# Optimization experiments

Measured on AMD Instinct MI355X. Metric: run time of the kernel, lower is better.

The kernel has to match this reference:

```python
import jax, jax.numpy as jnp
import numpy as np

N_NODES = 100000


def sage_conv(x, src, dst, w_self, w_neigh, b):
    # DGL SAGEConv with 'mean' aggregator: out = x @ W_self + mean_neigh(x) @ W_neigh + b
    msg = x[src]                                                     # [E, d] gather
    agg = jax.ops.segment_sum(msg, dst, num_segments=N_NODES)        # [N, d]
    deg = jax.ops.segment_sum(jnp.ones((src.shape[0],), x.dtype), dst,
                              num_segments=N_NODES)                  # [N]
    h_neigh = agg / jnp.maximum(deg, 1.0)[:, None]                   # mean; 0 for isolated nodes
    return x @ w_self + h_neigh @ w_neigh + b


def setup_inputs() -> dict:
    key = jax.random.key(0)
    ks = jax.random.split(key, 12)
    N, E = N_NODES, 1600000
    in_f, h_f, r_f = 128, 128, 64
    glorot = lambda k, i, o: jax.random.normal(k, (i, o), jnp.float32) / np.float32(np.sqrt(i))
    return {
        "in_feat": jax.random.normal(ks[0], (N, in_f), jnp.float32),
        "src": jax.random.randint(ks[1], (E,), 0, N),
        "dst": jax.random.randint(ks[2], (E,), 0, N),
        "w1_self": glorot(ks[3], in_f, h_f), "w1_neigh": glorot(ks[4], in_f, h_f), "b1": jnp.zeros((h_f,), jnp.float32),
        "w2_self": glorot(ks[5], h_f, r_f), "w2_neigh": glorot(ks[6], h_f, r_f), "b2": jnp.zeros((r_f,), jnp.float32),
        "w3_self": glorot(ks[7], r_f, r_f), "w3_neigh": glorot(ks[8], r_f, r_f), "b3": jnp.zeros((r_f,), jnp.float32),
    }


def reference(in_feat, src, dst,
              w1_self, w1_neigh, b1,
              w2_self, w2_neigh, b2,
              w3_self, w3_neigh, b3):
    h = sage_conv(in_feat, src, dst, w1_self, w1_neigh, b1)
    h = jax.nn.relu(h)
    h = sage_conv(h, src, dst, w2_self, w2_neigh, b2)
    h = jax.nn.relu(h)
    # dropout is treated as identity (deterministic eval-mode reference)
    h = sage_conv(h, src, dst, w3_self, w3_neigh, b3)
    return jax.nn.softmax(h, axis=-1)
```

## Files before the change

kernel.cpp:

```cpp
#include <hip/hip_runtime.h>
#include <hip/hip_bf16.h>

#define N_NODES 100000

typedef unsigned short ushort_t;
typedef __attribute__((ext_vector_type(8))) short short8;
typedef __attribute__((ext_vector_type(4))) float f32x4;

static __device__ __forceinline__ ushort_t f2bf(float f) {
    unsigned u = __float_as_uint(f);
    unsigned r = u + 0x7FFFu + ((u >> 16) & 1u);
    return (ushort_t)(r >> 16);
}
static __device__ __forceinline__ float bf2f(ushort_t h) {
    return __uint_as_float(((unsigned)h) << 16);
}

static __device__ __forceinline__ void split8(const float* __restrict__ xp,
                                              short8& hi, short8& lo) {
    float4 x0 = *(const float4*)xp;
    float4 x1 = *(const float4*)(xp + 4);
    float xs[8] = {x0.x, x0.y, x0.z, x0.w, x1.x, x1.y, x1.z, x1.w};
    #pragma unroll
    for (int j = 0; j < 8; ++j) {
        ushort_t h = f2bf(xs[j]);
        hi[j] = (short)h;
        lo[j] = (short)f2bf(xs[j] - bf2f(h));
    }
}

__global__ __launch_bounds__(256) void hist_kernel(const int* __restrict__ dst,
                                                   int* __restrict__ deg, int E) {
    int e = blockIdx.x * 256 + threadIdx.x;
    if (e < E) atomicAdd(&deg[__builtin_nontemporal_load(&dst[e])], 1);
}

__global__ __launch_bounds__(256) void scan_partial_sums(const int* __restrict__ deg,
                                                         int* __restrict__ partials, int N) {
    __shared__ int wsums[4];
    int tid = threadIdx.x, lane = tid & 63, wv = tid >> 6;
    int i0 = blockIdx.x * 1024 + tid * 4;
    int s = 0;
    #pragma unroll
    for (int j = 0; j < 4; ++j) {
        int i = i0 + j;
        if (i < N) s += deg[i];
    }
    #pragma unroll
    for (int off = 32; off > 0; off >>= 1) s += __shfl_xor(s, off, 64);
    if (lane == 0) wsums[wv] = s;
    __syncthreads();
    if (tid == 0)
        partials[blockIdx.x] = wsums[0] + wsums[1] + wsums[2] + wsums[3];
}

__global__ __launch_bounds__(256) void scan_partials(int* __restrict__ partials, int NB,
                                                     int* __restrict__ row_ptr, int N) {
    __shared__ int wsums[4];
    int tid = threadIdx.x, lane = tid & 63, wv = tid >> 6;
    int v = (tid < NB) ? partials[tid] : 0;
    int x = v;
    #pragma unroll
    for (int off = 1; off < 64; off <<= 1) {
        int y = __shfl_up(x, off, 64);
        if (lane >= off) x += y;
    }
    if (lane == 63) wsums[wv] = x;
    __syncthreads();
    int woff = 0;
    for (int w = 0; w < wv; ++w) woff += wsums[w];
    int incl = x + woff;
    if (tid < NB) partials[tid] = incl - v;
    if (tid == NB - 1) row_ptr[N] = incl;
}

__global__ __launch_bounds__(256) void scan_emit(const int* __restrict__ deg,
                                                 const int* __restrict__ partials,
                                                 int* __restrict__ row_ptr,
                                                 int* __restrict__ cursor,
                                                 float* __restrict__ inv_deg,
                                                 int* __restrict__ gcur, int N) {
    __shared__ int wsums[4];
    int tid = threadIdx.x, lane = tid & 63, wv = tid >> 6;
    int i0 = blockIdx.x * 1024 + tid * 4;
    int d[4];
    #pragma unroll
    for (int j = 0; j < 4; ++j) {
        int i = i0 + j;
        d[j] = (i < N) ? deg[i] : 0;
    }
    int s = d[0] + d[1] + d[2] + d[3];
    int x = s;
    #pragma unroll
    for (int off = 1; off < 64; off <<= 1) {
        int y = __shfl_up(x, off, 64);
        if (lane >= off) x += y;
    }
    if (lane == 63) wsums[wv] = x;
    __syncthreads();
    int woff = 0;
    for (int w = 0; w < wv; ++w) woff += wsums[w];
    int run = partials[blockIdx.x] + woff + x - s;
    #pragma unroll
    for (int j = 0; j < 4; ++j) {
        int i = i0 + j;
        if (i < N) {
            row_ptr[i] = run;
            cursor[i]  = run;
            inv_deg[i] = 1.0f / (float)(d[j] > 0 ? d[j] : 1);
            if ((i & 255) == 0) gcur[i >> 8] = run;
            run += d[j];
        }
    }
}

#define MAXBUCK 512
__global__ __launch_bounds__(256) void bin_pairs(const int* __restrict__ src,
                                                 const int* __restrict__ dst,
                                                 int* __restrict__ gcur,
                                                 long long* __restrict__ staged,
                                                 int E, int NBUCK, int C) {
    __shared__ int cnt[MAXBUCK];
    int tid = threadIdx.x;
    int e0 = blockIdx.x * C;
    int e1 = min(e0 + C, E);
    for (int b = tid; b < NBUCK; b += 256) cnt[b] = 0;
    __syncthreads();
    for (int e = e0 + tid; e < e1; e += 256) {
        int d = __builtin_nontemporal_load(&dst[e]);
        atomicAdd(&cnt[d >> 8], 1);
    }
    __syncthreads();
    for (int b = tid; b < NBUCK; b += 256) {
        int c = cnt[b];
        cnt[b] = (c > 0) ? atomicAdd(&gcur[b], c) : 0;
    }
    __syncthreads();
    for (int e = e0 + tid; e < e1; e += 256) {
        int d = __builtin_nontemporal_load(&dst[e]);
        int s = __builtin_nontemporal_load(&src[e]);
        int p = atomicAdd(&cnt[d >> 8], 1);
        staged[p] = ((long long)d << 32) | (unsigned)s;
    }
}

__global__ __launch_bounds__(256) void scatter_bucket(const long long* __restrict__ staged,
                                                      const int* __restrict__ row_ptr,
                                                      int* __restrict__ cursor,
                                                      int* __restrict__ edge_src,
                                                      int N) {
    int b = blockIdx.x;
    int lo = b << 8;
    int hiN = min((b + 1) << 8, N);
    int gstart = row_ptr[lo];
    int gend   = row_ptr[hiN];
    for (int p = gstart + threadIdx.x; p < gend; p += 256) {
        long long pr = __builtin_nontemporal_load(&staged[p]);
        int d = (int)(pr >> 32);
        int s = (int)(pr & 0xFFFFFFFFll);
        int pos = atomicAdd(&cursor[d], 1);
        edge_src[pos] = s;
    }
}

__global__ __launch_bounds__(256) void pack_all(
        const float* __restrict__ W0, const float* __restrict__ W1,
        const float* __restrict__ W2, const float* __restrict__ W3,
        const float* __restrict__ W4, const float* __restrict__ W5,
        ushort_t* H0, ushort_t* L0, ushort_t* H1, ushort_t* L1,
        ushort_t* H2, ushort_t* L2, ushort_t* H3, ushort_t* L3,
        ushort_t* H4, ushort_t* L4, ushort_t* H5, ushort_t* L5) {
    int b = blockIdx.x;
    const float* W; ushort_t* Hi; ushort_t* Lo; int K, NS, base;
    if (b < 8)       { W = W0; Hi = H0; Lo = L0; K = 128; NS = 128; base = 0;  }
    else if (b < 16) { W = W1; Hi = H1; Lo = L1; K = 128; NS = 128; base = 8;  }
    else if (b < 20) { W = W2; Hi = H2; Lo = L2; K = 128; NS = 64;  base = 16; }
    else if (b < 24) { W = W3; Hi = H3; Lo = L3; K = 128; NS = 64;  base = 20; }
    else if (b < 26) { W = W4; Hi = H4; Lo = L4; K = 64;  NS = 64;  base = 24; }
    else             { W = W5; Hi = H5; Lo = L5; K = 64;  NS = 64;  base = 26; }
    int tid = (b - base) * 256 + threadIdx.x;
    if (tid >= (K * NS) / 8) return;
    int l  = tid & 63;
    int fl = tid >> 6;
    int NT = NS / 16;
    int t = fl % NT, s = fl / NT;
    ushort_t hs[8], ls[8];
    #pragma unroll
    for (int j = 0; j < 8; ++j) {
        int k = s * 32 + (l >> 4) * 8 + j;
        int n = t * 16 + (l & 15);
        float w = W[(size_t)k * NS + n];
        ushort_t h = f2bf(w);
        hs[j] = h;
        ls[j] = f2bf(w - bf2f(h));
    }
    #pragma unroll
    for (int j = 0; j < 8; ++j) {
        Hi[(size_t)tid * 8 + j] = hs[j];
        Lo[(size_t)tid * 8 + j] = ls[j];
    }
}

template <int K, int NS>
__global__ __launch_bounds__(256) void mfma_gemm(const float* __restrict__ X,
                                                 const ushort_t* __restrict__ BsHi,
                                                 const ushort_t* __restrict__ BsLo,
                                                 const ushort_t* __restrict__ BnHi,
                                                 const ushort_t* __restrict__ BnLo,
                                                 const float* __restrict__ bias,
                                                 float* __restrict__ S,
                                                 ushort_t* __restrict__ Zb,
                                                 int M) {
    constexpr int KS = K / 32;
    constexpr int NT = NS / 16;
    __shared__ float ldsS[4][32 * 20];
    __shared__ float ldsZ[4][32 * 20];
    int tid = threadIdx.x;
    int lane = tid & 63, w = tid >> 6;
    int baseM = blockIdx.x * 128 + w * 32;
    int rIn = lane & 15, q = lane >> 4;
    float* bufS = ldsS[w];
    float* bufZ = ldsZ[w];

    short8 Ahi[KS][2], Alo[KS][2];
    #pragma unroll
    for (int s = 0; s < KS; ++s) {
        #pragma unroll
        for (int mt = 0; mt < 2; ++mt) {
            int gm = baseM + mt * 16 + rIn;
            if (gm < M) {
                split8(&X[(size_t)gm * K + s * 32 + q * 8], Ahi[s][mt], Alo[s][mt]);
            } else {
                #pragma unroll
                for (int j = 0; j < 8; ++j) { Ahi[s][mt][j] = 0; Alo[s][mt][j] = 0; }
            }
        }
    }

    for (int t = 0; t < NT; ++t) {
        f32x4 aS0 = {0.f, 0.f, 0.f, 0.f}, aS1 = {0.f, 0.f, 0.f, 0.f};
        f32x4 aZ0 = {0.f, 0.f, 0.f, 0.f}, aZ1 = {0.f, 0.f, 0.f, 0.f};
        #pragma unroll
        for (int s = 0; s < KS; ++s) {
            size_t fo = ((size_t)(s * NT + t) * 64 + lane) * 8;
            short8 bsh = *(const short8*)&BsHi[fo];
            short8 bsl = *(const short8*)&BsLo[fo];
            short8 bnh = *(const short8*)&BnHi[fo];
            short8 bnl = *(const short8*)&BnLo[fo];
            aS0 = __builtin_amdgcn_mfma_f32_16x16x32_bf16(Ahi[s][0], bsh, aS0, 0, 0, 0);
            aS0 = __builtin_amdgcn_mfma_f32_16x16x32_bf16(Alo[s][0], bsh, aS0, 0, 0, 0);
            aS0 = __builtin_amdgcn_mfma_f32_16x16x32_bf16(Ahi[s][0], bsl, aS0, 0, 0, 0);
            aS1 = __builtin_amdgcn_mfma_f32_16x16x32_bf16(Ahi[s][1], bsh, aS1, 0, 0, 0);
            aS1 = __builtin_amdgcn_mfma_f32_16x16x32_bf16(Alo[s][1], bsh, aS1, 0, 0, 0);
            aS1 = __builtin_amdgcn_mfma_f32_16x16x32_bf16(Ahi[s][1], bsl, aS1, 0, 0, 0);
            aZ0 = __builtin_amdgcn_mfma_f32_16x16x32_bf16(Ahi[s][0], bnh, aZ0, 0, 0, 0);
            aZ0 = __builtin_amdgcn_mfma_f32_16x16x32_bf16(Alo[s][0], bnh, aZ0, 0, 0, 0);
            aZ0 = __builtin_amdgcn_mfma_f32_16x16x32_bf16(Ahi[s][0], bnl, aZ0, 0, 0, 0);
            aZ1 = __builtin_amdgcn_mfma_f32_16x16x32_bf16(Ahi[s][1], bnh, aZ1, 0, 0, 0);
            aZ1 = __builtin_amdgcn_mfma_f32_16x16x32_bf16(Alo[s][1], bnh, aZ1, 0, 0, 0);
            aZ1 = __builtin_amdgcn_mfma_f32_16x16x32_bf16(Ahi[s][1], bnl, aZ1, 0, 0, 0);
        }
        #pragma unroll
        for (int r = 0; r < 4; ++r) {
            bufS[(q * 4 + r) * 20 + rIn]        = aS0[r];
            bufS[(16 + q * 4 + r) * 20 + rIn]   = aS1[r];
            bufZ[(q * 4 + r) * 20 + rIn]        = aZ0[r];
            bufZ[(16 + q * 4 + r) * 20 + rIn]   = aZ1[r];
        }
        int row = lane >> 2;
        int cq  = lane & 3;
        int col = t * 16 + cq * 4;
        float4 bv = *(const float4*)&bias[col];
        #pragma unroll
        for (int half = 0; half < 2; ++half) {
            int gm = baseM + half * 16 + row;
            float4 v = *(float4*)&bufS[(half * 16 + row) * 20 + cq * 4];
            float4 z = *(float4*)&bufZ[(half * 16 + row) * 20 + cq * 4];
            if (gm < M) {
                float4 o;
                o.x = v.x + bv.x; o.y = v.y + bv.y;
                o.z = v.z + bv.z; o.w = v.w + bv.w;
                *(float4*)&S[(size_t)gm * NS + col] = o;
                uint2 o2;
                o2.x = (unsigned)f2bf(z.x) | ((unsigned)f2bf(z.y) << 16);
                o2.y = (unsigned)f2bf(z.z) | ((unsigned)f2bf(z.w) << 16);
                *(uint2*)&Zb[(size_t)gm * NS + col] = o2;
            }
        }
    }
}

template <int D, int ACT>
__global__ __launch_bounds__(256) void agg_kernel(const float* __restrict__ S,
                                                  const uint2* __restrict__ Zu,
                                                  const int* __restrict__ row_ptr,
                                                  const int* __restrict__ edge_src,
                                                  const float* __restrict__ inv_deg,
                                                  float* __restrict__ out, int N) {
    constexpr int G  = D / 4;
    constexpr int NG = 256 / G;
    int tid = threadIdx.x;
    int g = tid / G, f4 = tid % G;
    int n = blockIdx.x * NG + g;
    if (n >= N) return;
    int beg = row_ptr[n], end = row_ptr[n + 1];

    float a0[4] = {0, 0, 0, 0}, a1[4] = {0, 0, 0, 0};
    float a2[4] = {0, 0, 0, 0}, a3[4] = {0, 0, 0, 0};
#define ACC(u, a)                                                              \
    a[0] += __uint_as_float((u).x << 16);                                      \
    a[1] += __uint_as_float((u).x & 0xFFFF0000u);                              \
    a[2] += __uint_as_float((u).y << 16);                                      \
    a[3] += __uint_as_float((u).y & 0xFFFF0000u);
    int j = beg;
    for (; j + 3 < end; j += 4) {
        int s0 = edge_src[j + 0], s1 = edge_src[j + 1];
        int s2 = edge_src[j + 2], s3 = edge_src[j + 3];
        uint2 u0 = Zu[(size_t)s0 * G + f4];
        uint2 u1 = Zu[(size_t)s1 * G + f4];
        uint2 u2 = Zu[(size_t)s2 * G + f4];
        uint2 u3 = Zu[(size_t)s3 * G + f4];
        ACC(u0, a0) ACC(u1, a1) ACC(u2, a2) ACC(u3, a3)
    }
    for (; j < end; ++j) {
        uint2 u = Zu[(size_t)edge_src[j] * G + f4];
        ACC(u, a0)
    }
#undef ACC
    float id = inv_deg[n];
    float4 sv = ((const float4*)(S + (size_t)n * D))[f4];
    float v[4];
    v[0] = sv.x + id * ((a0[0] + a1[0]) + (a2[0] + a3[0]));
    v[1] = sv.y + id * ((a0[1] + a1[1]) + (a2[1] + a3[1]));
    v[2] = sv.z + id * ((a0[2] + a1[2]) + (a2[2] + a3[2]));
    v[3] = sv.w + id * ((a0[3] + a1[3]) + (a2[3] + a3[3]));

    float4 o;
    if (ACT == 0) {
        o.x = fmaxf(v[0], 0.f); o.y = fmaxf(v[1], 0.f);
        o.z = fmaxf(v[2], 0.f); o.w = fmaxf(v[3], 0.f);
    } else {
        float m = fmaxf(fmaxf(v[0], v[1]), fmaxf(v[2], v[3]));
        #pragma unroll
        for (int off = 8; off > 0; off >>= 1) m = fmaxf(m, __shfl_xor(m, off, 16));
        float e0 = __expf(v[0] - m), e1 = __expf(v[1] - m);
        float e2 = __expf(v[2] - m), e3 = __expf(v[3] - m);
        float s = (e0 + e1) + (e2 + e3);
        #pragma unroll
        for (int off = 8; off > 0; off >>= 1) s += __shfl_xor(s, off, 16);
        float inv = 1.0f / s;
        o.x = e0 * inv; o.y = e1 * inv; o.z = e2 * inv; o.w = e3 * inv;
    }
    ((float4*)(out + (size_t)n * D))[f4] = o;
}

extern "C" void kernel_launch(void* const* d_in, const int* in_sizes, int n_in,
                              void* d_out, int out_size, void* d_ws, size_t ws_size,
                              hipStream_t stream) {
    const float* in_feat = (const float*)d_in[0];
    const int*   src     = (const int*)d_in[1];
    const int*   dst     = (const int*)d_in[2];
    const float* w1s = (const float*)d_in[3];
    const float* w1n = (const float*)d_in[4];
    const float* b1  = (const float*)d_in[5];
    const float* w2s = (const float*)d_in[6];
    const float* w2n = (const float*)d_in[7];
    const float* b2  = (const float*)d_in[8];
    const float* w3s = (const float*)d_in[9];
    const float* w3n = (const float*)d_in[10];
    const float* b3  = (const float*)d_in[11];

    const int N = N_NODES;
    const int E = in_sizes[1];

    char* p = (char*)d_ws;
    auto carve = [&](size_t bytes) -> char* {
        char* q = p;
        p += (bytes + 511) & ~(size_t)511;
        return q;
    };
    float*    S        = (float*)   carve((size_t)N * 128 * sizeof(float));
    ushort_t* Zb       = (ushort_t*)carve((size_t)N * 128 * sizeof(ushort_t));
    float*    H        = (float*)   carve((size_t)N * 128 * sizeof(float));
    int*      edge_src = (int*)     carve((size_t)E * sizeof(int));
    int*      row_ptr  = (int*)     carve((size_t)(N + 1) * sizeof(int));
    int*      cursor   = (int*)     carve((size_t)N * sizeof(int));
    int*      deg      = (int*)     carve((size_t)N * sizeof(int));
    float*    invd     = (float*)   carve((size_t)N * sizeof(float));
    int*      partials = (int*)     carve(256 * sizeof(int));
    int*      gcur     = (int*)     carve(MAXBUCK * sizeof(int));
    long long* staged  = (long long*)H;
    ushort_t* P1sH = (ushort_t*)carve(128 * 128 * 2); ushort_t* P1sL = (ushort_t*)carve(128 * 128 * 2);
    ushort_t* P1nH = (ushort_t*)carve(128 * 128 * 2); ushort_t* P1nL = (ushort_t*)carve(128 * 128 * 2);
    ushort_t* P2sH = (ushort_t*)carve(128 * 64 * 2);  ushort_t* P2sL = (ushort_t*)carve(128 * 64 * 2);
    ushort_t* P2nH = (ushort_t*)carve(128 * 64 * 2);  ushort_t* P2nL = (ushort_t*)carve(128 * 64 * 2);
    ushort_t* P3sH = (ushort_t*)carve(64 * 64 * 2);   ushort_t* P3sL = (ushort_t*)carve(64 * 64 * 2);
    ushort_t* P3nH = (ushort_t*)carve(64 * 64 * 2);   ushort_t* P3nL = (ushort_t*)carve(64 * 64 * 2);

    pack_all<<<28, 256, 0, stream>>>(w1s, w1n, w2s, w2n, w3s, w3n,
                                     P1sH, P1sL, P1nH, P1nL,
                                     P2sH, P2sL, P2nH, P2nL,
                                     P3sH, P3sL, P3nH, P3nL);

    (void)hipMemsetAsync(deg, 0, (size_t)N * sizeof(int), stream);
    hist_kernel<<<(E + 255) / 256, 256, 0, stream>>>(dst, deg, E);
    const int NB = (N + 1023) / 1024;
    scan_partial_sums<<<NB, 256, 0, stream>>>(deg, partials, N);
    scan_partials<<<1, 256, 0, stream>>>(partials, NB, row_ptr, N);
    scan_emit<<<NB, 256, 0, stream>>>(deg, partials, row_ptr, cursor, invd, gcur, N);
    const int NBUCK = (N + 255) >> 8;
    const int BINB  = 256;
    const int CHUNK = (E + BINB - 1) / BINB;
    bin_pairs<<<BINB, 256, 0, stream>>>(src, dst, gcur, staged, E, NBUCK, CHUNK);
    scatter_bucket<<<NBUCK, 256, 0, stream>>>(staged, row_ptr, cursor, edge_src, N);

    const int GB = (N + 127) / 128;

    mfma_gemm<128, 128><<<GB, 256, 0, stream>>>(in_feat, P1sH, P1sL, P1nH, P1nL, b1, S, Zb, N);
    agg_kernel<128, 0><<<(N + 7) / 8, 256, 0, stream>>>(S, (const uint2*)Zb,
                                                        row_ptr, edge_src, invd, H, N);

    mfma_gemm<128, 64><<<GB, 256, 0, stream>>>(H, P2sH, P2sL, P2nH, P2nL, b2, S, Zb, N);
    agg_kernel<64, 0><<<(N + 15) / 16, 256, 0, stream>>>(S, (const uint2*)Zb,
                                                         row_ptr, edge_src, invd, H, N);

    mfma_gemm<64, 64><<<GB, 256, 0, stream>>>(H, P3sH, P3sL, P3nH, P3nL, b3, S, Zb, N);
    agg_kernel<64, 1><<<(N + 15) / 16, 256, 0, stream>>>(S, (const uint2*)Zb,
                                                         row_ptr, edge_src, invd,
                                                         (float*)d_out, N);
}
```

Baseline: 474.6 us.

## Fuse setup kernels, store hidden activations in bf16, widen aggregation vectors

Merges weight packing with the degree histogram, and the bucket scatter with the first GEMM, into single launches so independent work shares one grid. Hidden activations between layers are now stored as bf16, and the later GEMMs use a single-term A operand (two MFMAs per tile instead of three), which cuts memory traffic and MFMA count. The aggregation kernel now reads 8 bf16 features per thread with uint4 loads and uses nontemporal loads for edge indices and S. The cost is lower precision on intermediate activations and a separate staging buffer that no longer aliases H.

```diff
diff --git a/kernel.cpp b/kernel.cpp
--- a/kernel.cpp
+++ b/kernel.cpp
@@ -29,10 +29,48 @@
     }
 }
 
-__global__ __launch_bounds__(256) void hist_kernel(const int* __restrict__ dst,
-                                                   int* __restrict__ deg, int E) {
-    int e = blockIdx.x * 256 + threadIdx.x;
-    if (e < E) atomicAdd(&deg[__builtin_nontemporal_load(&dst[e])], 1);
+__global__ __launch_bounds__(256) void pack_hist(
+        const float* __restrict__ W0, const float* __restrict__ W1,
+        const float* __restrict__ W2, const float* __restrict__ W3,
+        const float* __restrict__ W4, const float* __restrict__ W5,
+        ushort_t* H0, ushort_t* L0, ushort_t* H1, ushort_t* L1,
+        ushort_t* H2, ushort_t* L2, ushort_t* H3, ushort_t* L3,
+        ushort_t* H4, ushort_t* L4, ushort_t* H5, ushort_t* L5,
+        const int* __restrict__ dst, int* __restrict__ deg, int E) {
+    int b = blockIdx.x;
+    if (b >= 28) {
+        int e = (b - 28) * 256 + threadIdx.x;
+        if (e < E) atomicAdd(&deg[__builtin_nontemporal_load(&dst[e])], 1);
+        return;
+    }
+    const float* W; ushort_t* Hi; ushort_t* Lo; int K, NS, base;
+    if (b < 8)       { W = W0; Hi = H0; Lo = L0; K = 128; NS = 128; base = 0;  }
+    else if (b < 16) { W = W1; Hi = H1; Lo = L1; K = 128; NS = 128; base = 8;  }
+    else if (b < 20) { W = W2; Hi = H2; Lo = L2; K = 128; NS = 64;  base = 16; }
+    else if (b < 24) { W = W3; Hi = H3; Lo = L3; K = 128; NS = 64;  base = 20; }
+    else if (b < 26) { W = W4; Hi = H4; Lo = L4; K = 64;  NS = 64;  base = 24; }
+    else             { W = W5; Hi = H5; Lo = L5; K = 64;  NS = 64;  base = 26; }
+    int tid = (b - base) * 256 + threadIdx.x;
+    if (tid >= (K * NS) / 8) return;
+    int l  = tid & 63;
+    int fl = tid >> 6;
+    int NT = NS / 16;
+    int t = fl % NT, s = fl / NT;
+    ushort_t hs[8], ls[8];
+    #pragma unroll
+    for (int j = 0; j < 8; ++j) {
+        int k = s * 32 + (l >> 4) * 8 + j;
+        int n = t * 16 + (l & 15);
+        float w = W[(size_t)k * NS + n];
+        ushort_t h = f2bf(w);
+        hs[j] = h;
+        ls[j] = f2bf(w - bf2f(h));
+    }
+    #pragma unroll
+    for (int j = 0; j < 8; ++j) {
+        Hi[(size_t)tid * 8 + j] = hs[j];
+        Lo[(size_t)tid * 8 + j] = ls[j];
+    }
 }
 
 __global__ __launch_bounds__(256) void scan_partial_sums(const int* __restrict__ deg,
@@ -144,80 +182,38 @@
     }
 }
 
-__global__ __launch_bounds__(256) void scatter_bucket(const long long* __restrict__ staged,
-                                                      const int* __restrict__ row_ptr,
-                                                      int* __restrict__ cursor,
-                                                      int* __restrict__ edge_src,
-                                                      int N) {
-    int b = blockIdx.x;
-    int lo = b << 8;
-    int hiN = min((b + 1) << 8, N);
-    int gstart = row_ptr[lo];
-    int gend   = row_ptr[hiN];
-    for (int p = gstart + threadIdx.x; p < gend; p += 256) {
-        long long pr = __builtin_nontemporal_load(&staged[p]);
-        int d = (int)(pr >> 32);
-        int s = (int)(pr & 0xFFFFFFFFll);
-        int pos = atomicAdd(&cursor[d], 1);
-        edge_src[pos] = s;
-    }
-}
-
-__global__ __launch_bounds__(256) void pack_all(
-        const float* __restrict__ W0, const float* __restrict__ W1,
-        const float* __restrict__ W2, const float* __restrict__ W3,
-        const float* __restrict__ W4, const float* __restrict__ W5,
-        ushort_t* H0, ushort_t* L0, ushort_t* H1, ushort_t* L1,
-        ushort_t* H2, ushort_t* L2, ushort_t* H3, ushort_t* L3,
-        ushort_t* H4, ushort_t* L4, ushort_t* H5, ushort_t* L5) {
-    int b = blockIdx.x;
-    const float* W; ushort_t* Hi; ushort_t* Lo; int K, NS, base;
-    if (b < 8)       { W = W0; Hi = H0; Lo = L0; K = 128; NS = 128; base = 0;  }
-    else if (b < 16) { W = W1; Hi = H1; Lo = L1; K = 128; NS = 128; base = 8;  }
-    else if (b < 20) { W = W2; Hi = H2; Lo = L2; K = 128; NS = 64;  base = 16; }
-    else if (b < 24) { W = W3; Hi = H3; Lo = L3; K = 128; NS = 64;  base = 20; }
-    else if (b < 26) { W = W4; Hi = H4; Lo = L4; K = 64;  NS = 64;  base = 24; }
-    else             { W = W5; Hi = H5; Lo = L5; K = 64;  NS = 64;  base = 26; }
-    int tid = (b - base) * 256 + threadIdx.x;
-    if (tid >= (K * NS) / 8) return;
-    int l  = tid & 63;
-    int fl = tid >> 6;
-    int NT = NS / 16;
-    int t = fl % NT, s = fl / NT;
-    ushort_t hs[8], ls[8];
-    #pragma unroll
-    for (int j = 0; j < 8; ++j) {
-        int k = s * 32 + (l >> 4) * 8 + j;
-        int n = t * 16 + (l & 15);
-        float w = W[(size_t)k * NS + n];
-        ushort_t h = f2bf(w);
-        hs[j] = h;
-        ls[j] = f2bf(w - bf2f(h));
-    }
-    #pragma unroll
-    for (int j = 0; j < 8; ++j) {
-        Hi[(size_t)tid * 8 + j] = hs[j];
-        Lo[(size_t)tid * 8 + j] = ls[j];
-    }
-}
-
-template <int K, int NS>
-__global__ __launch_bounds__(256) void mfma_gemm(const float* __restrict__ X,
-                                                 const ushort_t* __restrict__ BsHi,
-                                                 const ushort_t* __restrict__ BsLo,
-                                                 const ushort_t* __restrict__ BnHi,
-                                                 const ushort_t* __restrict__ BnLo,
-                                                 const float* __restrict__ bias,
-                                                 float* __restrict__ S,
-                                                 ushort_t* __restrict__ Zb,
-                                                 int M) {
-    constexpr int KS = K / 32;
-    constexpr int NT = NS / 16;
+__global__ __launch_bounds__(256) void scatter_gemm1(
+        const long long* __restrict__ staged, const int* __restrict__ row_ptr,
+        int* __restrict__ cursor, int* __restrict__ edge_src, int NBUCK, int N,
+        const float* __restrict__ X,
+        const ushort_t* __restrict__ BsHi, const ushort_t* __restrict__ BsLo,
+        const ushort_t* __restrict__ BnHi, const ushort_t* __restrict__ BnLo,
+        const float* __restrict__ bias,
+        float* __restrict__ S, ushort_t* __restrict__ Zb, int M) {
+    constexpr int K = 128, NS = 128;
+    constexpr int KS = K / 32, NT = NS / 16;
     __shared__ float ldsS[4][32 * 20];
     __shared__ float ldsZ[4][32 * 20];
+
+    if ((int)blockIdx.x < NBUCK) {
+        int b = blockIdx.x;
+        int lo = b << 8;
+        int hiN = min((b + 1) << 8, N);
+        int gstart = row_ptr[lo];
+        int gend   = row_ptr[hiN];
+        for (int p = gstart + threadIdx.x; p < gend; p += 256) {
+            long long pr = __builtin_nontemporal_load(&staged[p]);
+            int d = (int)(pr >> 32);
+            int s = (int)(pr & 0xFFFFFFFFll);
+            int pos = atomicAdd(&cursor[d], 1);
+            edge_src[pos] = s;
+        }
+        return;
+    }
+    int bid = blockIdx.x - NBUCK;
     int tid = threadIdx.x;
     int lane = tid & 63, w = tid >> 6;
-    int baseM = blockIdx.x * 128 + w * 32;
+    int baseM = bid * 128 + w * 32;
     int rIn = lane & 15, q = lane >> 4;
     float* bufS = ldsS[w];
     float* bufZ = ldsZ[w];
@@ -262,10 +258,10 @@
         }
         #pragma unroll
         for (int r = 0; r < 4; ++r) {
-            bufS[(q * 4 + r) * 20 + rIn]        = aS0[r];
-            bufS[(16 + q * 4 + r) * 20 + rIn]   = aS1[r];
-            bufZ[(q * 4 + r) * 20 + rIn]        = aZ0[r];
-            bufZ[(16 + q * 4 + r) * 20 + rIn]   = aZ1[r];
+            bufS[(q * 4 + r) * 20 + rIn]      = aS0[r];
+            bufS[(16 + q * 4 + r) * 20 + rIn] = aS1[r];
+            bufZ[(q * 4 + r) * 20 + rIn]      = aZ0[r];
+            bufZ[(16 + q * 4 + r) * 20 + rIn] = aZ1[r];
         }
         int row = lane >> 2;
         int cq  = lane & 3;
@@ -290,68 +286,176 @@
     }
 }
 
-template <int D, int ACT>
+template <int K, int NS>
+__global__ __launch_bounds__(256) void mfma_gemm_bf16(const ushort_t* __restrict__ Xb,
+                                                      const ushort_t* __restrict__ BsHi,
+                                                      const ushort_t* __restrict__ BsLo,
+                                                      const ushort_t* __restrict__ BnHi,
+                                                      const ushort_t* __restrict__ BnLo,
+                                                      const float* __restrict__ bias,
+                                                      float* __restrict__ S,
+                                                      ushort_t* __restrict__ Zb,
+                                                      int M) {
+    constexpr int KS = K / 32, NT = NS / 16;
+    __shared__ float ldsS[4][32 * 20];
+    __shared__ float ldsZ[4][32 * 20];
+    int tid = threadIdx.x;
+    int lane = tid & 63, w = tid >> 6;
+    int baseM = blockIdx.x * 128 + w * 32;
+    int rIn = lane & 15, q = lane >> 4;
+    float* bufS = ldsS[w];
+    float* bufZ = ldsZ[w];
+
+    short8 A[KS][2];
+    #pragma unroll
+    for (int s = 0; s < KS; ++s) {
+        #pragma unroll
+        for (int mt = 0; mt < 2; ++mt) {
+            int gm = baseM + mt * 16 + rIn;
+            if (gm < M) {
+                A[s][mt] = *(const short8*)&Xb[(size_t)gm * K + s * 32 + q * 8];
+            } else {
+                #pragma unroll
+                for (int j = 0; j < 8; ++j) A[s][mt][j] = 0;
+            }
+        }
+    }
+
+    for (int t = 0; t < NT; ++t) {
+        f32x4 aS0 = {0.f, 0.f, 0.f, 0.f}, aS1 = {0.f, 0.f, 0.f, 0.f};
+        f32x4 aZ0 = {0.f, 0.f, 0.f, 0.f}, aZ1 = {0.f, 0.f, 0.f, 0.f};
+        #pragma unroll
+        for (int s = 0; s < KS; ++s) {
+            size_t fo = ((size_t)(s * NT + t) * 64 + lane) * 8;
+            short8 bsh = *(const short8*)&BsHi[fo];
+            short8 bsl = *(const short8*)&BsLo[fo];
+            short8 bnh = *(const short8*)&BnHi[fo];
+            short8 bnl = *(const short8*)&BnLo[fo];
+            aS0 = __builtin_amdgcn_mfma_f32_16x16x32_bf16(A[s][0], bsh, aS0, 0, 0, 0);
+            aS0 = __builtin_amdgcn_mfma_f32_16x16x32_bf16(A[s][0], bsl, aS0, 0, 0, 0);
+            aS1 = __builtin_amdgcn_mfma_f32_16x16x32_bf16(A[s][1], bsh, aS1, 0, 0, 0);
+            aS1 = __builtin_amdgcn_mfma_f32_16x16x32_bf16(A[s][1], bsl, aS1, 0, 0, 0);
+            aZ0 = __builtin_amdgcn_mfma_f32_16x16x32_bf16(A[s][0], bnh, aZ0, 0, 0, 0);
+            aZ0 = __builtin_amdgcn_mfma_f32_16x16x32_bf16(A[s][0], bnl, aZ0, 0, 0, 0);
+            aZ1 = __builtin_amdgcn_mfma_f32_16x16x32_bf16(A[s][1], bnh, aZ1, 0, 0, 0);
+            aZ1 = __builtin_amdgcn_mfma_f32_16x16x32_bf16(A[s][1], bnl, aZ1, 0, 0, 0);
+        }
+        #pragma unroll
+        for (int r = 0; r < 4; ++r) {
+            bufS[(q * 4 + r) * 20 + rIn]      = aS0[r];
+            bufS[(16 + q * 4 + r) * 20 + rIn] = aS1[r];
+            bufZ[(q * 4 + r) * 20 + rIn]      = aZ0[r];
+            bufZ[(16 + q * 4 + r) * 20 + rIn] = aZ1[r];
+        }
+        int row = lane >> 2;
+        int cq  = lane & 3;
+        int col = t * 16 + cq * 4;
+        float4 bv = *(const float4*)&bias[col];
+        #pragma unroll
+        for (int half = 0; half < 2; ++half) {
+            int gm = baseM + half * 16 + row;
+            float4 v = *(float4*)&bufS[(half * 16 + row) * 20 + cq * 4];
+            float4 z = *(float4*)&bufZ[(half * 16 + row) * 20 + cq * 4];
+            if (gm < M) {
+                float4 o;
+                o.x = v.x + bv.x; o.y = v.y + bv.y;
+                o.z = v.z + bv.z; o.w = v.w + bv.w;
+                *(float4*)&S[(size_t)gm * NS + col] = o;
+                uint2 o2;
+                o2.x = (unsigned)f2bf(z.x) | ((unsigned)f2bf(z.y) << 16);
+                o2.y = (unsigned)f2bf(z.z) | ((unsigned)f2bf(z.w) << 16);
+                *(uint2*)&Zb[(size_t)gm * NS + col] = o2;
+            }
+        }
+    }
+}
+
+template <int D, int ACT, int OUTBF>
 __global__ __launch_bounds__(256) void agg_kernel(const float* __restrict__ S,
-                                                  const uint2* __restrict__ Zu,
+                                                  const uint4* __restrict__ Zu,
                                                   const int* __restrict__ row_ptr,
                                                   const int* __restrict__ edge_src,
                                                   const float* __restrict__ inv_deg,
-                                                  float* __restrict__ out, int N) {
-    constexpr int G  = D / 4;
+                                                  void* __restrict__ outp, int N) {
+    constexpr int G  = D / 8;
     constexpr int NG = 256 / G;
     int tid = threadIdx.x;
-    int g = tid / G, f4 = tid % G;
+    int g = tid / G, f8 = tid % G;
     int n = blockIdx.x * NG + g;
     if (n >= N) return;
     int beg = row_ptr[n], end = row_ptr[n + 1];
 
-    float a0[4] = {0, 0, 0, 0}, a1[4] = {0, 0, 0, 0};
-    float a2[4] = {0, 0, 0, 0}, a3[4] = {0, 0, 0, 0};
-#define ACC(u, a)                                                              \
+    float a0[8] = {0,0,0,0,0,0,0,0}, a1[8] = {0,0,0,0,0,0,0,0};
+    float a2[8] = {0,0,0,0,0,0,0,0}, a3[8] = {0,0,0,0,0,0,0,0};
+#define ACC8(u, a)                                                             \
     a[0] += __uint_as_float((u).x << 16);                                      \
     a[1] += __uint_as_float((u).x & 0xFFFF0000u);                              \
     a[2] += __uint_as_float((u).y << 16);                                      \
-    a[3] += __uint_as_float((u).y & 0xFFFF0000u);
+    a[3] += __uint_as_float((u).y & 0xFFFF0000u);                              \
+    a[4] += __uint_as_float((u).z << 16);                                      \
+    a[5] += __uint_as_float((u).z & 0xFFFF0000u);                              \
+    a[6] += __uint_as_float((u).w << 16);                                      \
+    a[7] += __uint_as_float((u).w & 0xFFFF0000u);
     int j = beg;
     for (; j + 3 < end; j += 4) {
-        int s0 = edge_src[j + 0], s1 = edge_src[j + 1];
-        int s2 = edge_src[j + 2], s3 = edge_src[j + 3];
-        uint2 u0 = Zu[(size_t)s0 * G + f4];
-        uint2 u1 = Zu[(size_t)s1 * G + f4];
-        uint2 u2 = Zu[(size_t)s2 * G + f4];
-        uint2 u3 = Zu[(size_t)s3 * G + f4];
-        ACC(u0, a0) ACC(u1, a1) ACC(u2, a2) ACC(u3, a3)
+        int s0 = __builtin_nontemporal_load(&edge_src[j + 0]);
+        int s1 = __builtin_nontemporal_load(&edge_src[j + 1]);
+        int s2 = __builtin_nontemporal_load(&edge_src[j + 2]);
+        int s3 = __builtin_nontemporal_load(&edge_src[j + 3]);
+        uint4 u0 = Zu[(size_t)s0 * G + f8];
+        uint4 u1 = Zu[(size_t)s1 * G + f8];
+        uint4 u2 = Zu[(size_t)s2 * G + f8];
+        uint4 u3 = Zu[(size_t)s3 * G + f8];
+        ACC8(u0, a0) ACC8(u1, a1) ACC8(u2, a2) ACC8(u3, a3)
     }
     for (; j < end; ++j) {
-        uint2 u = Zu[(size_t)edge_src[j] * G + f4];
-        ACC(u, a0)
-    }
-#undef ACC
+        uint4 u = Zu[(size_t)__builtin_nontemporal_load(&edge_src[j]) * G + f8];
+        ACC8(u, a0)
+    }
+#undef ACC8
     float id = inv_deg[n];
-    float4 sv = ((const float4*)(S + (size_t)n * D))[f4];
-    float v[4];
-    v[0] = sv.x + id * ((a0[0] + a1[0]) + (a2[0] + a3[0]));
-    v[1] = sv.y + id * ((a0[1] + a1[1]) + (a2[1] + a3[1]));
-    v[2] = sv.z + id * ((a0[2] + a1[2]) + (a2[2] + a3[2]));
-    v[3] = sv.w + id * ((a0[3] + a1[3]) + (a2[3] + a3[3]));
-
-    float4 o;
+    f32x4 s0 = __builtin_nontemporal_load((const f32x4*)(S + (size_t)n * D + f8 * 8));
+    f32x4 s1 = __builtin_nontemporal_load((const f32x4*)(S + (size_t)n * D + f8 * 8 + 4));
+    float v[8];
+    #pragma unroll
+    for (int k = 0; k < 8; ++k) {
+        float sv = (k < 4) ? s0[k] : s1[k - 4];
+        v[k] = sv + id * ((a0[k] + a1[k]) + (a2[k] + a3[k]));
+    }
+
     if (ACT == 0) {
-        o.x = fmaxf(v[0], 0.f); o.y = fmaxf(v[1], 0.f);
-        o.z = fmaxf(v[2], 0.f); o.w = fmaxf(v[3], 0.f);
+        #pragma unroll
+        for (int k = 0; k < 8; ++k) v[k] = fmaxf(v[k], 0.f);
     } else {
-        float m = fmaxf(fmaxf(v[0], v[1]), fmaxf(v[2], v[3]));
-        #pragma unroll
-        for (int off = 8; off > 0; off >>= 1) m = fmaxf(m, __shfl_xor(m, off, 16));
-        float e0 = __expf(v[0] - m), e1 = __expf(v[1] - m);
-        float e2 = __expf(v[2] - m), e3 = __expf(v[3] - m);
-        float s = (e0 + e1) + (e2 + e3);
-        #pragma unroll
-        for (int off = 8; off > 0; off >>= 1) s += __shfl_xor(s, off, 16);
+        float m = v[0];
+        #pragma unroll
+        for (int k = 1; k < 8; ++k) m = fmaxf(m, v[k]);
+        #pragma unroll
+        for (int off = 4; off > 0; off >>= 1) m = fmaxf(m, __shfl_xor(m, off, 8));
+        float s = 0.f;
+        #pragma unroll
+        for (int k = 0; k < 8; ++k) { v[k] = __expf(v[k] - m); s += v[k]; }
+        #pragma unroll
+        for (int off = 4; off > 0; off >>= 1) s += __shfl_xor(s, off, 8);
         float inv = 1.0f / s;
-        o.x = e0 * inv; o.y = e1 * inv; o.z = e2 * inv; o.w = e3 * inv;
-    }
-    ((float4*)(out + (size_t)n * D))[f4] = o;
+        #pragma unroll
+        for (int k = 0; k < 8; ++k) v[k] *= inv;
+    }
+
+    if (OUTBF) {
+        uint4 o;
+        o.x = (unsigned)f2bf(v[0]) | ((unsigned)f2bf(v[1]) << 16);
+        o.y = (unsigned)f2bf(v[2]) | ((unsigned)f2bf(v[3]) << 16);
+        o.z = (unsigned)f2bf(v[4]) | ((unsigned)f2bf(v[5]) << 16);
+        o.w = (unsigned)f2bf(v[6]) | ((unsigned)f2bf(v[7]) << 16);
+        ((uint4*)((ushort_t*)outp + (size_t)n * D))[f8] = o;
+    } else {
+        float4 o0 = make_float4(v[0], v[1], v[2], v[3]);
+        float4 o1 = make_float4(v[4], v[5], v[6], v[7]);
+        float* po = (float*)outp + (size_t)n * D + f8 * 8;
+        *(float4*)po = o0;
+        *(float4*)(po + 4) = o1;
+    }
 }
 
 extern "C" void kernel_launch(void* const* d_in, const int* in_sizes, int n_in,
@@ -381,7 +485,7 @@
     };
     float*    S        = (float*)   carve((size_t)N * 128 * sizeof(float));
     ushort_t* Zb       = (ushort_t*)carve((size_t)N * 128 * sizeof(ushort_t));
-    float*    H        = (float*)   carve((size_t)N * 128 * sizeof(float));
+    ushort_t* Hb       = (ushort_t*)carve((size_t)N * 128 * sizeof(ushort_t));
     int*      edge_src = (int*)     carve((size_t)E * sizeof(int));
     int*      row_ptr  = (int*)     carve((size_t)(N + 1) * sizeof(int));
     int*      cursor   = (int*)     carve((size_t)N * sizeof(int));
@@ -389,7 +493,7 @@
     float*    invd     = (float*)   carve((size_t)N * sizeof(float));
     int*      partials = (int*)     carve(256 * sizeof(int));
     int*      gcur     = (int*)     carve(MAXBUCK * sizeof(int));
-    long long* staged  = (long long*)H;
+    long long* staged  = (long long*)carve((size_t)E * sizeof(long long));
     ushort_t* P1sH = (ushort_t*)carve(128 * 128 * 2); ushort_t* P1sL = (ushort_t*)carve(128 * 128 * 2);
     ushort_t* P1nH = (ushort_t*)carve(128 * 128 * 2); ushort_t* P1nL = (ushort_t*)carve(128 * 128 * 2);
     ushort_t* P2sH = (ushort_t*)carve(128 * 64 * 2);  ushort_t* P2sL = (ushort_t*)carve(128 * 64 * 2);
@@ -397,35 +501,37 @@
     ushort_t* P3sH = (ushort_t*)carve(64 * 64 * 2);   ushort_t* P3sL = (ushort_t*)carve(64 * 64 * 2);
     ushort_t* P3nH = (ushort_t*)carve(64 * 64 * 2);   ushort_t* P3nL = (ushort_t*)carve(64 * 64 * 2);
 
-    pack_all<<<28, 256, 0, stream>>>(w1s, w1n, w2s, w2n, w3s, w3n,
-                                     P1sH, P1sL, P1nH, P1nL,
-                                     P2sH, P2sL, P2nH, P2nL,
-                                     P3sH, P3sL, P3nH, P3nL);
+    const int NBUCK = (N + 255) >> 8;
+    const int GB    = (N + 127) / 128;
+    const int NB    = (N + 1023) / 1024;
 
     (void)hipMemsetAsync(deg, 0, (size_t)N * sizeof(int), stream);
-    hist_kernel<<<(E + 255) / 256, 256, 0, stream>>>(dst, deg, E);
-    const int NB = (N + 1023) / 1024;
+    pack_hist<<<28 + (E + 255) / 256, 256, 0, stream>>>(
+        w1s, w1n, w2s, w2n, w3s, w3n,
+        P1sH, P1sL, P1nH, P1nL, P2sH, P2sL, P2nH, P2nL, P3sH, P3sL, P3nH, P3nL,
+        dst, deg, E);
+
     scan_partial_sums<<<NB, 256, 0, stream>>>(deg, partials, N);
     scan_partials<<<1, 256, 0, stream>>>(partials, NB, row_ptr, N);
     scan_emit<<<NB, 256, 0, stream>>>(deg, partials, row_ptr, cursor, invd, gcur, N);
-    const int NBUCK = (N + 255) >> 8;
     const int BINB  = 256;
     const int CHUNK = (E + BINB - 1) / BINB;
     bin_pairs<<<BINB, 256, 0, stream>>>(src, dst, gcur, staged, E, NBUCK, CHUNK);
-    scatter_bucket<<<NBUCK, 256, 0, stream>>>(staged, row_ptr, cursor, edge_src, N);
-
-    const int GB = (N + 127) / 128;
-
-    mfma_gemm<128, 128><<<GB, 256, 0, stream>>>(in_feat, P1sH, P1sL, P1nH, P1nL, b1, S, Zb, N);
-    agg_kernel<128, 0><<<(N + 7) / 8, 256, 0, stream>>>(S, (const uint2*)Zb,
-                                                        row_ptr, edge_src, invd, H, N);
-
-    mfma_gemm<128, 64><<<GB, 256, 0, stream>>>(H, P2sH, P2sL, P2nH, P2nL, b2, S, Zb, N);
-    agg_kernel<64, 0><<<(N + 15) / 16, 256, 0, stream>>>(S, (const uint2*)Zb,
-                                                         row_ptr, edge_src, invd, H, N);
-
-    mfma_gemm<64, 64><<<GB, 256, 0, stream>>>(H, P3sH, P3sL, P3nH, P3nL, b3, S, Zb, N);
-    agg_kernel<64, 1><<<(N + 15) / 16, 256, 0, stream>>>(S, (const uint2*)Zb,
-                                                         row_ptr, edge_src, invd,
-                                                         (float*)d_out, N);
-}
+
+    scatter_gemm1<<<NBUCK + GB, 256, 0, stream>>>(staged, row_ptr, cursor, edge_src,
+                                                  NBUCK, N,
+                                                  in_feat, P1sH, P1sL, P1nH, P1nL,
+                                                  b1, S, Zb, N);
+    agg_kernel<128, 0, 1><<<(N + 15) / 16, 256, 0, stream>>>(
+        S, (const uint4*)Zb, row_ptr, edge_src, invd, Hb, N);
+
+    mfma_gemm_bf16<128, 64><<<GB, 256, 0, stream>>>(Hb, P2sH, P2sL, P2nH, P2nL,
+                                                    b2, S, Zb, N);
+    agg_kernel<64, 0, 1><<<(N + 31) / 32, 256, 0, stream>>>(
+        S, (const uint4*)Zb, row_ptr, edge_src, invd, Hb, N);
+
+    mfma_gemm_bf16<64, 64><<<GB, 256, 0, stream>>>(Hb, P3sH, P3sL, P3nH, P3nL,
+                                                   b3, S, Zb, N);
+    agg_kernel<64, 1, 0><<<(N + 31) / 32, 256, 0, stream>>>(
+        S, (const uint4*)Zb, row_ptr, edge_src, invd, d_out, N);
+}
```

Result: no change. 475.1 us (+0.1%).
